# Kernel optimization log

Measured on AMD Instinct MI355X. Metric: run time of the kernel, lower is better.

## Reference

```python
import jax, jax.numpy as jnp
import numpy as np

B, S, HID = 2, 2048, 1024
H, D = 16, HID // 16  # heads, head_dim
ROPE_BASE = 10000.0


def setup_inputs() -> dict:
    key = jax.random.key(0)
    k1, k2, k3, k4 = jax.random.split(key, 4)
    scale = 1.0 / np.sqrt(HID)
    return {
        "hidden_states": jax.random.normal(k1, (B, S, HID), dtype=jnp.float32),
        "attention_mask": jnp.zeros((B, 1, 1, S), dtype=jnp.float32),
        "Wq": jax.random.normal(k2, (HID, HID), dtype=jnp.float32) * scale,
        "Wk": jax.random.normal(k3, (HID, HID), dtype=jnp.float32) * scale,
        "Wv": jax.random.normal(k4, (HID, HID), dtype=jnp.float32) * scale,
    }


def _rope_cos_sin(seq_len, dim, dtype):
    inv_freq = 1.0 / (ROPE_BASE ** (jnp.arange(0, dim, 2, dtype=jnp.float32) / dim))
    freqs = jnp.arange(seq_len, dtype=jnp.float32)[:, None] * inv_freq[None, :]  # (S, D/2)
    emb = jnp.concatenate([freqs, freqs], axis=-1)  # (S, D)
    return jnp.cos(emb).astype(dtype), jnp.sin(emb).astype(dtype)


def _rotate_half(x):
    x1, x2 = jnp.split(x, 2, axis=-1)
    return jnp.concatenate([-x2, x1], axis=-1)


def reference(hidden_states, attention_mask, Wq, Wk, Wv):
    b, s, _ = hidden_states.shape
    # QKV projections (no bias), split into heads: (b, H, s, D)
    def proj(W):
        return jnp.einsum('bse,de->bsd', hidden_states, W).reshape(b, s, H, D).transpose(0, 2, 1, 3)
    q, k, v = proj(Wq), proj(Wk), proj(Wv)
    # Rotary embedding on q, k over sequence positions
    cos, sin = _rope_cos_sin(s, D, hidden_states.dtype)  # (s, D)
    cos = cos[None, None]  # (1,1,s,D)
    sin = sin[None, None]
    q = q * cos + _rotate_half(q) * sin
    k = k * cos + _rotate_half(k) * sin
    # Scaled dot-product attention with additive mask
    scores = jnp.einsum('bhqd,bhkd->bhqk', q, k) / jnp.sqrt(jnp.asarray(D, hidden_states.dtype))
    scores = scores + attention_mask
    probs = jax.nn.softmax(scores, axis=-1)  # dropout p=0 (eval) -> identity
    ctx = jnp.einsum('bhqk,bhkd->bhqd', probs, v)
    return ctx.transpose(0, 2, 1, 3).reshape(b, s, H * D)
```

## Files before the change

### kernel.cpp

```cpp
#include <hip/hip_runtime.h>
#include <stdint.h>

typedef unsigned short u16;
typedef short bf16x8 __attribute__((ext_vector_type(8)));
typedef float f32x4 __attribute__((ext_vector_type(4)));

#define S_ 2048
#define HID_ 1024
#define H_ 16
#define D_ 64

#define LOG2E 1.4426950408889634f
#define SCALE_LOG2 0.18033688011112042f
#define MAXC_LOG2 11.541560327111707f

__device__ __forceinline__ u16 f2bf(float f) {
  uint32_t x = __builtin_bit_cast(uint32_t, f);
  uint32_t r = (x + 0x7fffu + ((x >> 16) & 1u)) >> 16;
  return (u16)r;
}
__device__ __forceinline__ uint32_t packbf2(float a, float b) {
  return (uint32_t)f2bf(a) | ((uint32_t)f2bf(b) << 16);
}
__device__ __forceinline__ uint32_t permpack(float a, float b) {
  return __builtin_amdgcn_perm(__builtin_bit_cast(uint32_t, b),
                               __builtin_bit_cast(uint32_t, a), 0x07060302u);
}

__device__ __forceinline__ void gl2lds16(const void* g, void* l) {
  __builtin_amdgcn_global_load_lds(
      (const __attribute__((address_space(1))) unsigned int*)g,
      (__attribute__((address_space(3))) unsigned int*)l, 16, 0, 0);
}

#define NX_ (1 << 20)
#define NW_ (1 << 18)
#define NROPE_ 65536
__global__ void prep_kernel(const float* __restrict__ X, const float* __restrict__ Wq,
                            const float* __restrict__ Wk, const float* __restrict__ Wv,
                            const float* __restrict__ mask, u16* __restrict__ Xb,
                            u16* __restrict__ Wqb, u16* __restrict__ Wkb,
                            u16* __restrict__ Wvb, float* __restrict__ cos_t,
                            float* __restrict__ sin_t, float* __restrict__ mask2) {
  int i = blockIdx.x * 256 + threadIdx.x;
  if (i < NX_ + 3 * NW_) {
    const float* src;
    u16* dst;
    int off;
    if (i < NX_) {
      src = X; dst = Xb; off = i;
    } else if (i < NX_ + NW_) {
      src = Wq; dst = Wqb; off = i - NX_;
    } else if (i < NX_ + 2 * NW_) {
      src = Wk; dst = Wkb; off = i - NX_ - NW_;
    } else {
      src = Wv; dst = Wvb; off = i - NX_ - 2 * NW_;
    }
    float4 v = ((const float4*)src)[off];
    uint2 packed;
    packed.x = packbf2(v.x, v.y);
    packed.y = packbf2(v.z, v.w);
    ((uint2*)dst)[off] = packed;
  } else if (i < NX_ + 3 * NW_ + NROPE_) {
    int t = i - (NX_ + 3 * NW_);
    int s = t >> 5, j = t & 31;
    float invf = powf(10000.0f, -(float)j * (1.0f / 32.0f));
    float ang = (float)s * invf;
    cos_t[t] = cosf(ang);
    sin_t[t] = sinf(ang);
  } else {
    int t = i - (NX_ + 3 * NW_ + NROPE_);
    mask2[t] = fmaf(mask[t], LOG2E, -MAXC_LOG2);
  }
}

__global__ __launch_bounds__(256) void qkv_gemm_kernel(
    const u16* __restrict__ X, const u16* __restrict__ Wq, const u16* __restrict__ Wk,
    const u16* __restrict__ Wv, const float* __restrict__ cos_t,
    const float* __restrict__ sin_t, u16* __restrict__ Q, u16* __restrict__ K,
    u16* __restrict__ Vt) {
  __shared__ char smem[65536];
  int tid = threadIdx.x;
  int lane = tid & 63, wave = tid >> 6;
  int wm = wave >> 1, wn = wave & 1;
  int quad = lane >> 4, l16 = lane & 15;
  int which = blockIdx.x >> 3;
  int nbase = (blockIdx.x & 7) * 128;
  int mbase = blockIdx.y * 128;
  const u16* W = (which == 0) ? Wq : (which == 1) ? Wk : Wv;

#pragma unroll
  for (int it = 0; it < 4; ++it) {
    int i = it * 256 + tid;
    int r = i >> 3, gs = i & 7, gsrc = gs ^ (r & 7);
    gl2lds16(X + (size_t)(mbase + r) * HID_ + gsrc * 8, smem + i * 16);
    gl2lds16(W + (size_t)(nbase + r) * HID_ + gsrc * 8, smem + 32768 + i * 16);
  }

  f32x4 acc[4][4] = {};

  for (int kk = 0; kk < 16; ++kk) {
    char* As = smem + (kk & 1) * 16384;
    char* Bs = smem + 32768 + (kk & 1) * 16384;
    __syncthreads();

    if (kk < 15) {
      int k0n = (kk + 1) * 64;
      char* An = smem + ((kk + 1) & 1) * 16384;
      char* Bn = smem + 32768 + ((kk + 1) & 1) * 16384;
#pragma unroll
      for (int it = 0; it < 4; ++it) {
        int i = it * 256 + tid;
        int r = i >> 3, gs = i & 7, gsrc = gs ^ (r & 7);
        gl2lds16(X + (size_t)(mbase + r) * HID_ + k0n + gsrc * 8, An + i * 16);
        gl2lds16(W + (size_t)(nbase + r) * HID_ + k0n + gsrc * 8, Bn + i * 16);
      }
    }

#pragma unroll
    for (int kh = 0; kh < 2; ++kh) {
      bf16x8 afrag[4], bfrag[4];
#pragma unroll
      for (int i4 = 0; i4 < 4; ++i4) {
        int r = wm * 64 + i4 * 16 + l16;
        int L = r * 8 + ((kh * 4 + quad) ^ (r & 7));
        afrag[i4] = *(const bf16x8*)(As + L * 16);
      }
#pragma unroll
      for (int j4 = 0; j4 < 4; ++j4) {
        int r = wn * 64 + j4 * 16 + l16;
        int L = r * 8 + ((kh * 4 + quad) ^ (r & 7));
        bfrag[j4] = *(const bf16x8*)(Bs + L * 16);
      }
      if (which == 2) {
#pragma unroll
        for (int i4 = 0; i4 < 4; ++i4)
#pragma unroll
          for (int j4 = 0; j4 < 4; ++j4)
            acc[i4][j4] = __builtin_amdgcn_mfma_f32_16x16x32_bf16(afrag[i4], bfrag[j4],
                                                                  acc[i4][j4], 0, 0, 0);
      } else {
#pragma unroll
        for (int i4 = 0; i4 < 4; ++i4)
#pragma unroll
          for (int j4 = 0; j4 < 4; ++j4)
            acc[i4][j4] = __builtin_amdgcn_mfma_f32_16x16x32_bf16(bfrag[j4], afrag[i4],
                                                                  acc[i4][j4], 0, 0, 0);
      }
    }
  }

  if (which == 2) {
#pragma unroll
    for (int i4 = 0; i4 < 4; ++i4)
#pragma unroll
      for (int j4 = 0; j4 < 4; ++j4) {
        int m = mbase + wm * 64 + i4 * 16 + quad * 4;
        int n = nbase + wn * 64 + j4 * 16 + l16;
        int b = m >> 11, s0 = m & 2047;
        int h = n >> 6, d = n & 63;
        uint2 pk;
        pk.x = packbf2(acc[i4][j4][0], acc[i4][j4][1]);
        pk.y = packbf2(acc[i4][j4][2], acc[i4][j4][3]);
        *(uint2*)(Vt + (((size_t)(b * H_ + h)) * D_ + d) * S_ + s0) = pk;
      }
  } else {
    u16* dst = (which == 0) ? Q : K;
#pragma unroll
    for (int i4 = 0; i4 < 4; ++i4)
#pragma unroll
      for (int j4 = 0; j4 < 2; ++j4) {
        int m = mbase + wm * 64 + i4 * 16 + l16;
        int n1 = nbase + wn * 64 + j4 * 16 + quad * 4;
        int b = m >> 11, s = m & 2047;
        int h = n1 >> 6, d1 = n1 & 63;
        float4 c4 = *(const float4*)(cos_t + s * 32 + d1);
        float4 s4 = *(const float4*)(sin_t + s * 32 + d1);
        float y1[4], y2[4];
#pragma unroll
        for (int r = 0; r < 4; ++r) {
          float cr = ((const float*)&c4)[r], sr = ((const float*)&s4)[r];
          float x1 = acc[i4][j4][r], x2 = acc[i4][j4 + 2][r];
          y1[r] = x1 * cr - x2 * sr;
          y2[r] = x2 * cr + x1 * sr;
        }
        size_t base = ((size_t)(b * H_ + h) * S_ + s) * D_;
        uint2 p1, p2;
        p1.x = packbf2(y1[0], y1[1]);
        p1.y = packbf2(y1[2], y1[3]);
        p2.x = packbf2(y2[0], y2[1]);
        p2.y = packbf2(y2[2], y2[3]);
        *(uint2*)(dst + base + d1) = p1;
        *(uint2*)(dst + base + d1 + 32) = p2;
      }
  }
}

__device__ __forceinline__ void pv_step(const char* Pr, const char* Vp, int quad, int l16,
                                        const bf16x8& ones, f32x4* o0, f32x4* o1,
                                        f32x4& lacc0, f32x4& lacc1) {
  bf16x8 p0[2], p1[2];
#pragma unroll
  for (int kh = 0; kh < 2; ++kh) {
    int c0 = kh * 8 + quad * 2;
    union { uint2 u[2]; bf16x8 v; } cv0, cv1;
    cv0.u[0] = *(const uint2*)(Pr + l16 * 128 + ((c0) ^ l16) * 8);
    cv0.u[1] = *(const uint2*)(Pr + l16 * 128 + ((c0 + 1) ^ l16) * 8);
    cv1.u[0] = *(const uint2*)(Pr + 2048 + l16 * 128 + ((c0) ^ l16) * 8);
    cv1.u[1] = *(const uint2*)(Pr + 2048 + l16 * 128 + ((c0 + 1) ^ l16) * 8);
    p0[kh] = cv0.v;
    p1[kh] = cv1.v;
  }
  lacc0 = __builtin_amdgcn_mfma_f32_16x16x32_bf16(p0[0], ones, lacc0, 0, 0, 0);
  lacc0 = __builtin_amdgcn_mfma_f32_16x16x32_bf16(p0[1], ones, lacc0, 0, 0, 0);
  lacc1 = __builtin_amdgcn_mfma_f32_16x16x32_bf16(p1[0], ones, lacc1, 0, 0, 0);
  lacc1 = __builtin_amdgcn_mfma_f32_16x16x32_bf16(p1[1], ones, lacc1, 0, 0, 0);
#pragma unroll
  for (int jd = 0; jd < 4; ++jd) {
    int r = jd * 16 + l16;
#pragma unroll
    for (int kh = 0; kh < 2; ++kh) {
      int L = r * 8 + ((kh * 4 + quad) ^ (r & 7));
      bf16x8 vf = *(const bf16x8*)(Vp + L * 16);
      o0[jd] = __builtin_amdgcn_mfma_f32_16x16x32_bf16(p0[kh], vf, o0[jd], 0, 0, 0);
      o1[jd] = __builtin_amdgcn_mfma_f32_16x16x32_bf16(p1[kh], vf, o1[jd], 0, 0, 0);
    }
  }
}

__global__ __launch_bounds__(256) void flash_kernel(
    const u16* __restrict__ Q, const u16* __restrict__ K, const u16* __restrict__ Vt,
    const float* __restrict__ mask2, float* __restrict__ out) {
  __shared__ char smem[81920];
  int tid = threadIdx.x, wave = tid >> 6;
  int lane = tid & 63;
  int quad = lane >> 4, l16 = lane & 15;
  int bh = blockIdx.y, b = bh >> 4, h = bh & 15;
  int qbase = blockIdx.x * 128;
  int qw = qbase + wave * 32;
  const float* m2row = mask2 + b * S_;
  const u16* Kbase = K + (size_t)bh * S_ * D_;
  const u16* Vbase = Vt + (size_t)bh * D_ * S_;

  bf16x8 qfrag[2][2];
#pragma unroll
  for (int g = 0; g < 2; ++g) {
    const u16* qp = Q + ((size_t)bh * S_ + qw + g * 16 + l16) * D_ + quad * 8;
    qfrag[g][0] = *(const bf16x8*)qp;
    qfrag[g][1] = *(const bf16x8*)(qp + 32);
  }
  bf16x8 ones;
#pragma unroll
  for (int j = 0; j < 8; ++j) ones[j] = (short)0x3f80;

  f32x4 o0[4] = {}, o1[4] = {};
  f32x4 lacc0 = {}, lacc1 = {};

#pragma unroll
  for (int it = 0; it < 2; ++it) {
    int i = it * 256 + tid;
    int r = i >> 3, gs = i & 7, gsrc = gs ^ (r & 7);
    gl2lds16(Kbase + (size_t)r * D_ + gsrc * 8, smem + i * 16);
    gl2lds16(Vbase + (size_t)r * S_ + gsrc * 8, smem + 8192 + i * 16);
  }
  float4 mv[4];
#pragma unroll
  for (int jt = 0; jt < 4; ++jt) mv[jt] = *(const float4*)(m2row + jt * 16 + quad * 4);

  for (int kt = 0; kt < 32; ++kt) {
    char* Ks = smem + (kt % 3) * 16384;
    __syncthreads();

    if (kt < 31) {
      char* Kn = smem + ((kt + 1) % 3) * 16384;
      char* Vn = Kn + 8192;
      int nb = (kt + 1) * 64;
#pragma unroll
      for (int it = 0; it < 2; ++it) {
        int i = it * 256 + tid;
        int r = i >> 3, gs = i & 7, gsrc = gs ^ (r & 7);
        gl2lds16(Kbase + (size_t)(nb + r) * D_ + gsrc * 8, Kn + i * 16);
        gl2lds16(Vbase + (size_t)r * S_ + nb + gsrc * 8, Vn + i * 16);
      }
    }

    if (kt > 0) {
      const char* Pr = smem + 49152 + ((kt - 1) & 1) * 16384 + wave * 4096;
      const char* Vp = smem + ((kt - 1) % 3) * 16384 + 8192;
      pv_step(Pr, Vp, quad, l16, ones, o0, o1, lacc0, lacc1);
    }

    f32x4 s0[4] = {}, s1[4] = {};
#pragma unroll
    for (int jt = 0; jt < 4; ++jt) {
      int r = jt * 16 + l16;
#pragma unroll
      for (int kh = 0; kh < 2; ++kh) {
        int L = r * 8 + ((kh * 4 + quad) ^ (r & 7));
        bf16x8 kf = *(const bf16x8*)(Ks + L * 16);
        s0[jt] = __builtin_amdgcn_mfma_f32_16x16x32_bf16(kf, qfrag[0][kh], s0[jt], 0, 0, 0);
        s1[jt] = __builtin_amdgcn_mfma_f32_16x16x32_bf16(kf, qfrag[1][kh], s1[jt], 0, 0, 0);
      }
    }

    char* Pwb = smem + 49152 + (kt & 1) * 16384 + wave * 4096;
#pragma unroll
    for (int jt = 0; jt < 4; ++jt) {
      float p0f[4], p1f[4];
#pragma unroll
      for (int r = 0; r < 4; ++r) {
        float mvr = ((const float*)&mv[jt])[r];
        p0f[r] = __builtin_amdgcn_exp2f(fmaf(s0[jt][r], SCALE_LOG2, mvr));
        p1f[r] = __builtin_amdgcn_exp2f(fmaf(s1[jt][r], SCALE_LOG2, mvr));
      }
      uint2 pk0, pk1;
      pk0.x = permpack(p0f[0], p0f[1]);
      pk0.y = permpack(p0f[2], p0f[3]);
      pk1.x = permpack(p1f[0], p1f[1]);
      pk1.y = permpack(p1f[2], p1f[3]);
      int chunk = (jt * 4 + quad) ^ l16;
      *(uint2*)(Pwb + l16 * 128 + chunk * 8) = pk0;
      *(uint2*)(Pwb + 2048 + l16 * 128 + chunk * 8) = pk1;
    }

    if (kt < 31) {
#pragma unroll
      for (int jt = 0; jt < 4; ++jt)
        mv[jt] = *(const float4*)(m2row + (kt + 1) * 64 + jt * 16 + quad * 4);
    }
  }

  {
    const char* Pr = smem + 49152 + 16384 + wave * 4096;
    const char* Vp = smem + 16384 + 8192;
    pv_step(Pr, Vp, quad, l16, ones, o0, o1, lacc0, lacc1);
  }

  float inv0[4], inv1[4];
#pragma unroll
  for (int r = 0; r < 4; ++r) {
    inv0[r] = 1.0f / lacc0[r];
    inv1[r] = 1.0f / lacc1[r];
  }
#pragma unroll
  for (int jd = 0; jd < 4; ++jd) {
#pragma unroll
    for (int r = 0; r < 4; ++r) {
      int d = jd * 16 + l16;
      int q0 = qw + quad * 4 + r;
      out[(((size_t)b * S_ + q0) * H_ + h) * D_ + d] = o0[jd][r] * inv0[r];
      int q1 = qw + 16 + quad * 4 + r;
      out[(((size_t)b * S_ + q1) * H_ + h) * D_ + d] = o1[jd][r] * inv1[r];
    }
  }
}

extern "C" void kernel_launch(void* const* d_in, const int* in_sizes, int n_in,
                              void* d_out, int out_size, void* d_ws, size_t ws_size,
                              hipStream_t stream) {
  const float* hid = (const float*)d_in[0];
  const float* mask = (const float*)d_in[1];
  const float* Wq = (const float*)d_in[2];
  const float* Wk = (const float*)d_in[3];
  const float* Wv = (const float*)d_in[4];
  float* out = (float*)d_out;
  char* ws = (char*)d_ws;

  u16* Xbf = (u16*)ws;
  u16* Wqb = (u16*)(ws + (8u << 20));
  u16* Wkb = (u16*)(ws + (10u << 20));
  u16* Wvb = (u16*)(ws + (12u << 20));
  u16* Qb = (u16*)(ws + (14u << 20));
  u16* Kb = (u16*)(ws + (22u << 20));
  u16* Vtb = (u16*)(ws + (30u << 20));
  float* cos_t = (float*)(ws + (38u << 20));
  float* sin_t = (float*)(ws + (38u << 20) + (256u << 10));
  float* mask2 = (float*)(ws + (38u << 20) + (512u << 10));

  prep_kernel<<<7440, 256, 0, stream>>>(hid, Wq, Wk, Wv, mask, Xbf, Wqb, Wkb, Wvb,
                                        cos_t, sin_t, mask2);
  qkv_gemm_kernel<<<dim3(24, 32), 256, 0, stream>>>(Xbf, Wqb, Wkb, Wvb, cos_t, sin_t,
                                                    Qb, Kb, Vtb);
  flash_kernel<<<dim3(16, 32), 256, 0, stream>>>(Qb, Kb, Vtb, mask2, out);
}
```

Before: 178.0 us.

## Split flash attention work across eight waves of sixteen queries each

The attention kernel now launches 512 threads per block, with each wave handling 16 query rows instead of 32. The aim is more waves per CU to hide latency, fewer accumulator registers per thread, and a per-thread K/V tile load split of one chunk instead of two. The P scratch buffer becomes single-buffered per wave, which shrinks shared memory to 64KB. In exchange, each K/V fragment read from LDS feeds only one MFMA instead of two, which raises LDS traffic per unit of math. The tighter launch bound also risks register spills.

```diff
diff --git a/kernel.cpp b/kernel.cpp
--- a/kernel.cpp
+++ b/kernel.cpp
@@ -197,24 +197,18 @@
 }
 
 __device__ __forceinline__ void pv_step(const char* Pr, const char* Vp, int quad, int l16,
-                                        const bf16x8& ones, f32x4* o0, f32x4* o1,
-                                        f32x4& lacc0, f32x4& lacc1) {
-  bf16x8 p0[2], p1[2];
+                                        const bf16x8& ones, f32x4* o, f32x4& lacc) {
+  bf16x8 p[2];
 #pragma unroll
   for (int kh = 0; kh < 2; ++kh) {
     int c0 = kh * 8 + quad * 2;
-    union { uint2 u[2]; bf16x8 v; } cv0, cv1;
-    cv0.u[0] = *(const uint2*)(Pr + l16 * 128 + ((c0) ^ l16) * 8);
-    cv0.u[1] = *(const uint2*)(Pr + l16 * 128 + ((c0 + 1) ^ l16) * 8);
-    cv1.u[0] = *(const uint2*)(Pr + 2048 + l16 * 128 + ((c0) ^ l16) * 8);
-    cv1.u[1] = *(const uint2*)(Pr + 2048 + l16 * 128 + ((c0 + 1) ^ l16) * 8);
-    p0[kh] = cv0.v;
-    p1[kh] = cv1.v;
-  }
-  lacc0 = __builtin_amdgcn_mfma_f32_16x16x32_bf16(p0[0], ones, lacc0, 0, 0, 0);
-  lacc0 = __builtin_amdgcn_mfma_f32_16x16x32_bf16(p0[1], ones, lacc0, 0, 0, 0);
-  lacc1 = __builtin_amdgcn_mfma_f32_16x16x32_bf16(p1[0], ones, lacc1, 0, 0, 0);
-  lacc1 = __builtin_amdgcn_mfma_f32_16x16x32_bf16(p1[1], ones, lacc1, 0, 0, 0);
+    union { uint2 u[2]; bf16x8 v; } cv;
+    cv.u[0] = *(const uint2*)(Pr + l16 * 128 + ((c0) ^ l16) * 8);
+    cv.u[1] = *(const uint2*)(Pr + l16 * 128 + ((c0 + 1) ^ l16) * 8);
+    p[kh] = cv.v;
+  }
+  lacc = __builtin_amdgcn_mfma_f32_16x16x32_bf16(p[0], ones, lacc, 0, 0, 0);
+  lacc = __builtin_amdgcn_mfma_f32_16x16x32_bf16(p[1], ones, lacc, 0, 0, 0);
 #pragma unroll
   for (int jd = 0; jd < 4; ++jd) {
     int r = jd * 16 + l16;
@@ -222,43 +216,41 @@
     for (int kh = 0; kh < 2; ++kh) {
       int L = r * 8 + ((kh * 4 + quad) ^ (r & 7));
       bf16x8 vf = *(const bf16x8*)(Vp + L * 16);
-      o0[jd] = __builtin_amdgcn_mfma_f32_16x16x32_bf16(p0[kh], vf, o0[jd], 0, 0, 0);
-      o1[jd] = __builtin_amdgcn_mfma_f32_16x16x32_bf16(p1[kh], vf, o1[jd], 0, 0, 0);
-    }
-  }
-}
-
-__global__ __launch_bounds__(256) void flash_kernel(
+      o[jd] = __builtin_amdgcn_mfma_f32_16x16x32_bf16(p[kh], vf, o[jd], 0, 0, 0);
+    }
+  }
+}
+
+__global__ __launch_bounds__(512, 4) void flash_kernel(
     const u16* __restrict__ Q, const u16* __restrict__ K, const u16* __restrict__ Vt,
     const float* __restrict__ mask2, float* __restrict__ out) {
-  __shared__ char smem[81920];
+  __shared__ char smem[65536];
   int tid = threadIdx.x, wave = tid >> 6;
   int lane = tid & 63;
   int quad = lane >> 4, l16 = lane & 15;
   int bh = blockIdx.y, b = bh >> 4, h = bh & 15;
   int qbase = blockIdx.x * 128;
-  int qw = qbase + wave * 32;
+  int qw = qbase + wave * 16;
+  char* Pw = smem + 49152 + wave * 2048;
   const float* m2row = mask2 + b * S_;
   const u16* Kbase = K + (size_t)bh * S_ * D_;
   const u16* Vbase = Vt + (size_t)bh * D_ * S_;
 
-  bf16x8 qfrag[2][2];
-#pragma unroll
-  for (int g = 0; g < 2; ++g) {
-    const u16* qp = Q + ((size_t)bh * S_ + qw + g * 16 + l16) * D_ + quad * 8;
-    qfrag[g][0] = *(const bf16x8*)qp;
-    qfrag[g][1] = *(const bf16x8*)(qp + 32);
+  bf16x8 qfrag[2];
+  {
+    const u16* qp = Q + ((size_t)bh * S_ + qw + l16) * D_ + quad * 8;
+    qfrag[0] = *(const bf16x8*)qp;
+    qfrag[1] = *(const bf16x8*)(qp + 32);
   }
   bf16x8 ones;
 #pragma unroll
   for (int j = 0; j < 8; ++j) ones[j] = (short)0x3f80;
 
-  f32x4 o0[4] = {}, o1[4] = {};
-  f32x4 lacc0 = {}, lacc1 = {};
-
-#pragma unroll
-  for (int it = 0; it < 2; ++it) {
-    int i = it * 256 + tid;
+  f32x4 o[4] = {};
+  f32x4 lacc = {};
+
+  {
+    int i = tid;
     int r = i >> 3, gs = i & 7, gsrc = gs ^ (r & 7);
     gl2lds16(Kbase + (size_t)r * D_ + gsrc * 8, smem + i * 16);
     gl2lds16(Vbase + (size_t)r * S_ + gsrc * 8, smem + 8192 + i * 16);
@@ -275,22 +267,18 @@
       char* Kn = smem + ((kt + 1) % 3) * 16384;
       char* Vn = Kn + 8192;
       int nb = (kt + 1) * 64;
-#pragma unroll
-      for (int it = 0; it < 2; ++it) {
-        int i = it * 256 + tid;
-        int r = i >> 3, gs = i & 7, gsrc = gs ^ (r & 7);
-        gl2lds16(Kbase + (size_t)(nb + r) * D_ + gsrc * 8, Kn + i * 16);
-        gl2lds16(Vbase + (size_t)r * S_ + nb + gsrc * 8, Vn + i * 16);
-      }
+      int i = tid;
+      int r = i >> 3, gs = i & 7, gsrc = gs ^ (r & 7);
+      gl2lds16(Kbase + (size_t)(nb + r) * D_ + gsrc * 8, Kn + i * 16);
+      gl2lds16(Vbase + (size_t)r * S_ + nb + gsrc * 8, Vn + i * 16);
     }
 
     if (kt > 0) {
-      const char* Pr = smem + 49152 + ((kt - 1) & 1) * 16384 + wave * 4096;
       const char* Vp = smem + ((kt - 1) % 3) * 16384 + 8192;
-      pv_step(Pr, Vp, quad, l16, ones, o0, o1, lacc0, lacc1);
-    }
-
-    f32x4 s0[4] = {}, s1[4] = {};
+      pv_step(Pw, Vp, quad, l16, ones, o, lacc);
+    }
+
+    f32x4 s[4] = {};
 #pragma unroll
     for (int jt = 0; jt < 4; ++jt) {
       int r = jt * 16 + l16;
@@ -298,29 +286,23 @@
       for (int kh = 0; kh < 2; ++kh) {
         int L = r * 8 + ((kh * 4 + quad) ^ (r & 7));
         bf16x8 kf = *(const bf16x8*)(Ks + L * 16);
-        s0[jt] = __builtin_amdgcn_mfma_f32_16x16x32_bf16(kf, qfrag[0][kh], s0[jt], 0, 0, 0);
-        s1[jt] = __builtin_amdgcn_mfma_f32_16x16x32_bf16(kf, qfrag[1][kh], s1[jt], 0, 0, 0);
-      }
-    }
-
-    char* Pwb = smem + 49152 + (kt & 1) * 16384 + wave * 4096;
+        s[jt] = __builtin_amdgcn_mfma_f32_16x16x32_bf16(kf, qfrag[kh], s[jt], 0, 0, 0);
+      }
+    }
+
 #pragma unroll
     for (int jt = 0; jt < 4; ++jt) {
-      float p0f[4], p1f[4];
+      float pf[4];
 #pragma unroll
       for (int r = 0; r < 4; ++r) {
         float mvr = ((const float*)&mv[jt])[r];
-        p0f[r] = __builtin_amdgcn_exp2f(fmaf(s0[jt][r], SCALE_LOG2, mvr));
-        p1f[r] = __builtin_amdgcn_exp2f(fmaf(s1[jt][r], SCALE_LOG2, mvr));
-      }
-      uint2 pk0, pk1;
-      pk0.x = permpack(p0f[0], p0f[1]);
-      pk0.y = permpack(p0f[2], p0f[3]);
-      pk1.x = permpack(p1f[0], p1f[1]);
-      pk1.y = permpack(p1f[2], p1f[3]);
+        pf[r] = __builtin_amdgcn_exp2f(fmaf(s[jt][r], SCALE_LOG2, mvr));
+      }
+      uint2 pk;
+      pk.x = permpack(pf[0], pf[1]);
+      pk.y = permpack(pf[2], pf[3]);
       int chunk = (jt * 4 + quad) ^ l16;
-      *(uint2*)(Pwb + l16 * 128 + chunk * 8) = pk0;
-      *(uint2*)(Pwb + 2048 + l16 * 128 + chunk * 8) = pk1;
+      *(uint2*)(Pw + l16 * 128 + chunk * 8) = pk;
     }
 
     if (kt < 31) {
@@ -330,27 +312,18 @@
     }
   }
 
-  {
-    const char* Pr = smem + 49152 + 16384 + wave * 4096;
-    const char* Vp = smem + 16384 + 8192;
-    pv_step(Pr, Vp, quad, l16, ones, o0, o1, lacc0, lacc1);
-  }
-
-  float inv0[4], inv1[4];
-#pragma unroll
-  for (int r = 0; r < 4; ++r) {
-    inv0[r] = 1.0f / lacc0[r];
-    inv1[r] = 1.0f / lacc1[r];
-  }
+  pv_step(Pw, smem + 16384 + 8192, quad, l16, ones, o, lacc);
+
+  float inv[4];
+#pragma unroll
+  for (int r = 0; r < 4; ++r) inv[r] = 1.0f / lacc[r];
 #pragma unroll
   for (int jd = 0; jd < 4; ++jd) {
 #pragma unroll
     for (int r = 0; r < 4; ++r) {
       int d = jd * 16 + l16;
-      int q0 = qw + quad * 4 + r;
-      out[(((size_t)b * S_ + q0) * H_ + h) * D_ + d] = o0[jd][r] * inv0[r];
-      int q1 = qw + 16 + quad * 4 + r;
-      out[(((size_t)b * S_ + q1) * H_ + h) * D_ + d] = o1[jd][r] * inv1[r];
+      int q = qw + quad * 4 + r;
+      out[(((size_t)b * S_ + q) * H_ + h) * D_ + d] = o[jd][r] * inv[r];
     }
   }
 }
@@ -381,5 +354,5 @@
                                         cos_t, sin_t, mask2);
   qkv_gemm_kernel<<<dim3(24, 32), 256, 0, stream>>>(Xbf, Wqb, Wkb, Wvb, cos_t, sin_t,
                                                     Qb, Kb, Vtb);
-  flash_kernel<<<dim3(16, 32), 256, 0, stream>>>(Qb, Kb, Vtb, mask2, out);
-}
+  flash_kernel<<<dim3(16, 32), 512, 0, stream>>>(Qb, Kb, Vtb, mask2, out);
+}
```

Measured after the change: 171.0 us. 1.04x faster.
